# Kernel optimization log

Hardware: AMD Instinct MI355X
Metric: run time of the kernel (lower is better)

## Reference

```python
import jax, jax.numpy as jnp
import numpy as np

B, N, C, L, E = 8, 8192, 256, 4, 131072  # graphs, nodes/graph, channels (in=hidden=out), layers, edges/graph


def setup_inputs() -> dict:
    key = jax.random.key(0)
    ks = jax.random.split(key, 9)
    batch_node_tsr = jax.random.normal(ks[0], (B, N, C), jnp.float32)
    edge_index = jax.random.randint(ks[1], (B, 2, E), 0, N, jnp.int32)
    batch_last_node_idx_list = jnp.arange(1, B + 1, dtype=jnp.int32) * N - 1
    s1 = 1.0 / np.sqrt(C)
    s2 = 1.0 / np.sqrt(2 * C)
    # Base GraphConv layers: out = x @ Wr.T + sum_nbr(x) @ Wn.T + b  (all CxC since in=hidden=out)
    base_Wr = jax.random.uniform(ks[2], (L, C, C), jnp.float32, -s1, s1)
    base_Wn = jax.random.uniform(ks[3], (L, C, C), jnp.float32, -s1, s1)
    base_b = jax.random.uniform(ks[4], (L, C), jnp.float32, -s1, s1)
    # Adapter GraphConv layers take concatenated (2C) input
    adapt_Wr = jax.random.uniform(ks[5], (L, C, 2 * C), jnp.float32, -s2, s2)
    adapt_Wn = jax.random.uniform(ks[6], (L, C, 2 * C), jnp.float32, -s2, s2)
    adapt_b = jax.random.uniform(ks[7], (L, C), jnp.float32, -s2, s2)
    return dict(batch_node_tsr=batch_node_tsr, base_Wr=base_Wr, base_Wn=base_Wn,
                base_b=base_b, adapt_Wr=adapt_Wr, adapt_Wn=adapt_Wn, adapt_b=adapt_b,
                edge_index=edge_index, batch_last_node_idx_list=batch_last_node_idx_list)


def reference(batch_node_tsr, base_Wr, base_Wn, base_b, adapt_Wr, adapt_Wn, adapt_b,
              edge_index, batch_last_node_idx_list):
    # Batch graphs PyG-style: offset per-graph node indices into one big graph
    offsets = (jnp.arange(B, dtype=edge_index.dtype) * N)[:, None]  # [B,1]
    src = (edge_index[:, 0, :] + offsets).reshape(-1)  # [B*E]
    dst = (edge_index[:, 1, :] + offsets).reshape(-1)  # [B*E]
    x = batch_node_tsr.reshape(B * N, C)

    def gconv(h, Wr, Wn, b):
        # GraphConv: root transform + sum-aggregated neighbor transform
        agg = jax.ops.segment_sum(h[src], dst, num_segments=B * N)
        return h @ Wr.T + agg @ Wn.T + b

    # Base encoder pass, keeping all latent embeds
    lat = [x]
    for i in range(L):
        lat.append(jax.nn.relu(gconv(lat[-1], base_Wr[i], base_Wn[i], base_b[i])))
    base_batch_embed = lat[-1].reshape(B, N, C)

    # Adapter pass: concat(base_latent[i+1], curr) -> adapter GraphConv -> relu
    curr = x
    for i in range(L):
        curr = jax.nn.relu(gconv(jnp.concatenate([lat[i + 1], curr], axis=-1),
                                 adapt_Wr[i], adapt_Wn[i], adapt_b[i]))
    adapter_batch_embed = curr.reshape(B, N, C)
    return base_batch_embed, adapter_batch_embed
```

## Files before the change

kernel.cpp:

```cpp
#include <hip/hip_runtime.h>

#define B_ 8
#define N_ 8192
#define C_ 256
#define L_ 4
#define E_ 131072
#define BN_ 65536
#define EDGES_ 1048576
#define NKEY_ (BN_ * 4)

typedef __attribute__((ext_vector_type(8))) short short8;
typedef __attribute__((ext_vector_type(4))) float f32x4;

__device__ __forceinline__ unsigned short f2bf(float f){
  unsigned int u = __builtin_bit_cast(unsigned int, f);
  u += 0x7fffu + ((u >> 16) & 1u);
  return (unsigned short)(u >> 16);
}
__device__ __forceinline__ float bf2f(unsigned short h){
  unsigned int u = ((unsigned int)h) << 16;
  return __builtin_bit_cast(float, u);
}

__launch_bounds__(256)
__global__ void cvt_bf16_k(const float* __restrict__ in, unsigned short* __restrict__ out, int n4){
  int t = blockIdx.x * 256 + threadIdx.x;
  if (t >= n4) return;
  float4 v = ((const float4*)in)[t];
  ushort4 o;
  o.x = f2bf(v.x); o.y = f2bf(v.y); o.z = f2bf(v.z); o.w = f2bf(v.w);
  ((ushort4*)out)[t] = o;
}

__launch_bounds__(256)
__global__ void hist_k(const int* __restrict__ ei, int* __restrict__ cnt){
  int t = blockIdx.x * 256 + threadIdx.x;
  int b = t >> 17, e = t & (E_ - 1);
  int src = ei[b * (2 * E_) + e];
  int dst = ei[b * (2 * E_) + E_ + e];
  int key = (((b << 13) + dst) << 2) | (src >> 11);
  atomicAdd(&cnt[key], 1);
}

__launch_bounds__(256)
__global__ void scanA_k(const int* __restrict__ cnt, int* __restrict__ bsum){
  __shared__ int ls[256];
  int b = blockIdx.x, t = threadIdx.x;
  int4 v = *(const int4*)(cnt + b * 1024 + t * 4);
  int s = v.x + v.y + v.z + v.w;
  ls[t] = s;
  __syncthreads();
  for (int d = 128; d > 0; d >>= 1){
    if (t < d) ls[t] += ls[t + d];
    __syncthreads();
  }
  if (t == 0) bsum[b] = ls[0];
}
__launch_bounds__(256)
__global__ void scanB_k(const int* __restrict__ bsum, int* __restrict__ boff){
  __shared__ int ls[256];
  int t = threadIdx.x;
  int v = bsum[t];
  ls[t] = v;
  __syncthreads();
  for (int d = 1; d < 256; d <<= 1){
    int x = (t >= d) ? ls[t - d] : 0;
    __syncthreads();
    ls[t] += x;
    __syncthreads();
  }
  boff[t] = ls[t] - v;
}
__launch_bounds__(256)
__global__ void scanC_k(const int* __restrict__ cnt, const int* __restrict__ boff,
                        int* __restrict__ row_ptr, int* __restrict__ cursor){
  __shared__ int ls[256];
  int b = blockIdx.x, t = threadIdx.x;
  int base = b * 1024 + t * 4;
  int4 v = *(const int4*)(cnt + base);
  int s = v.x + v.y + v.z + v.w;
  ls[t] = s;
  __syncthreads();
  for (int d = 1; d < 256; d <<= 1){
    int x = (t >= d) ? ls[t - d] : 0;
    __syncthreads();
    ls[t] += x;
    __syncthreads();
  }
  int off = boff[b] + ls[t] - s;
  int4 rp;
  rp.x = off;
  rp.y = off + v.x;
  rp.z = rp.y + v.y;
  rp.w = rp.z + v.z;
  *(int4*)(row_ptr + base) = rp;
  *(int4*)(cursor + base) = rp;
  if (b == 255 && t == 255) row_ptr[NKEY_] = EDGES_;
}

__launch_bounds__(256)
__global__ void scat_k(const int* __restrict__ ei, int* __restrict__ cursor, int* __restrict__ col){
  int t = blockIdx.x * 256 + threadIdx.x;
  int b = t >> 17, e = t & (E_ - 1);
  int src = ei[b * (2 * E_) + e];
  int dst = ei[b * (2 * E_) + E_ + e];
  int key = (((b << 13) + dst) << 2) | (src >> 11);
  int pos = atomicAdd(&cursor[key], 1);
  col[pos] = (b << 13) + src;
}

__launch_bounds__(256)
__global__ void agg_k(const unsigned short* __restrict__ feat, const int* __restrict__ row_ptr,
                      const int* __restrict__ col, unsigned short* __restrict__ out){
  int w = threadIdx.x >> 6, lane = threadIdx.x & 63;
  int g = blockIdx.x & 7, sblk = blockIdx.x >> 3;
  int node = (g << 13) + (sblk << 2) + w;
  int beg = row_ptr[node << 2], end = row_ptr[(node << 2) + 4];
  int ch = lane << 2;
  float a0=0,a1=0,a2=0,a3=0;
  int e = beg;
  for (; e + 4 <= end; e += 4){
    int s0 = __builtin_nontemporal_load(col + e);
    int s1 = __builtin_nontemporal_load(col + e + 1);
    int s2 = __builtin_nontemporal_load(col + e + 2);
    int s3 = __builtin_nontemporal_load(col + e + 3);
    ushort4 v0 = *(const ushort4*)(feat + ((size_t)s0 << 8) + ch);
    ushort4 v1 = *(const ushort4*)(feat + ((size_t)s1 << 8) + ch);
    ushort4 v2 = *(const ushort4*)(feat + ((size_t)s2 << 8) + ch);
    ushort4 v3 = *(const ushort4*)(feat + ((size_t)s3 << 8) + ch);
    a0 += (bf2f(v0.x) + bf2f(v1.x)) + (bf2f(v2.x) + bf2f(v3.x));
    a1 += (bf2f(v0.y) + bf2f(v1.y)) + (bf2f(v2.y) + bf2f(v3.y));
    a2 += (bf2f(v0.z) + bf2f(v1.z)) + (bf2f(v2.z) + bf2f(v3.z));
    a3 += (bf2f(v0.w) + bf2f(v1.w)) + (bf2f(v2.w) + bf2f(v3.w));
  }
  for (; e < end; ++e){
    int s0 = __builtin_nontemporal_load(col + e);
    ushort4 v0 = *(const ushort4*)(feat + ((size_t)s0 << 8) + ch);
    a0 += bf2f(v0.x); a1 += bf2f(v0.y); a2 += bf2f(v0.z); a3 += bf2f(v0.w);
  }
  ushort4 o;
  o.x = f2bf(a0); o.y = f2bf(a1); o.z = f2bf(a2); o.w = f2bf(a3);
  unsigned long long ov = __builtin_bit_cast(unsigned long long, o);
  __builtin_nontemporal_store(ov, (unsigned long long*)(out + ((size_t)node << 8) + ch));
}

__launch_bounds__(256)
__global__ void agg2_k(const unsigned short* __restrict__ fA, const unsigned short* __restrict__ fB,
                       const int* __restrict__ row_ptr, const int* __restrict__ col,
                       unsigned short* __restrict__ oA, unsigned short* __restrict__ oB){
  int w = threadIdx.x >> 6, lane = threadIdx.x & 63;
  int g = blockIdx.x & 7, sblk = blockIdx.x >> 3;
  int node = (g << 13) + (sblk << 2) + w;
  int beg = row_ptr[node << 2], end = row_ptr[(node << 2) + 4];
  int ch = lane << 2;
  float a0=0,a1=0,a2=0,a3=0, c0=0,c1=0,c2=0,c3=0;
  int e = beg;
  for (; e + 2 <= end; e += 2){
    int s0 = __builtin_nontemporal_load(col + e);
    int s1 = __builtin_nontemporal_load(col + e + 1);
    ushort4 va0 = *(const ushort4*)(fA + ((size_t)s0 << 8) + ch);
    ushort4 vb0 = *(const ushort4*)(fB + ((size_t)s0 << 8) + ch);
    ushort4 va1 = *(const ushort4*)(fA + ((size_t)s1 << 8) + ch);
    ushort4 vb1 = *(const ushort4*)(fB + ((size_t)s1 << 8) + ch);
    a0 += bf2f(va0.x) + bf2f(va1.x); a1 += bf2f(va0.y) + bf2f(va1.y);
    a2 += bf2f(va0.z) + bf2f(va1.z); a3 += bf2f(va0.w) + bf2f(va1.w);
    c0 += bf2f(vb0.x) + bf2f(vb1.x); c1 += bf2f(vb0.y) + bf2f(vb1.y);
    c2 += bf2f(vb0.z) + bf2f(vb1.z); c3 += bf2f(vb0.w) + bf2f(vb1.w);
  }
  if (e < end){
    int s0 = __builtin_nontemporal_load(col + e);
    ushort4 va0 = *(const ushort4*)(fA + ((size_t)s0 << 8) + ch);
    ushort4 vb0 = *(const ushort4*)(fB + ((size_t)s0 << 8) + ch);
    a0 += bf2f(va0.x); a1 += bf2f(va0.y); a2 += bf2f(va0.z); a3 += bf2f(va0.w);
    c0 += bf2f(vb0.x); c1 += bf2f(vb0.y); c2 += bf2f(vb0.z); c3 += bf2f(vb0.w);
  }
  ushort4 oa, ob;
  oa.x = f2bf(a0); oa.y = f2bf(a1); oa.z = f2bf(a2); oa.w = f2bf(a3);
  ob.x = f2bf(c0); ob.y = f2bf(c1); ob.z = f2bf(c2); ob.w = f2bf(c3);
  unsigned long long va = __builtin_bit_cast(unsigned long long, oa);
  unsigned long long vb = __builtin_bit_cast(unsigned long long, ob);
  __builtin_nontemporal_store(va, (unsigned long long*)(oA + ((size_t)node << 8) + ch));
  __builtin_nontemporal_store(vb, (unsigned long long*)(oB + ((size_t)node << 8) + ch));
}

#define GLDS16(gp, lp) __builtin_amdgcn_global_load_lds( \
    (const __attribute__((address_space(1))) void*)(gp), \
    (__attribute__((address_space(3))) void*)(lp), 16, 0, 0)

__device__ __forceinline__ void stage_tiles(const unsigned short* __restrict__ A,
                                            const unsigned short* __restrict__ W,
                                            int ldw, int k0, unsigned short* a_t, int t){
  unsigned short* b_t = a_t + 4096;
#pragma unroll
  for (int c = t; c < 512; c += 256){
    int row = c >> 2, seg = c & 3;
    int sg = seg ^ ((row >> 1) & 3);
    GLDS16(A + row * C_  + k0 + sg * 8, &a_t[c * 8]);
  }
#pragma unroll
  for (int c = t; c < 1024; c += 256){
    int row = c >> 2, seg = c & 3;
    int sg = seg ^ ((row >> 1) & 3);
    GLDS16(W + row * ldw + k0 + sg * 8, &b_t[c * 8]);
  }
}

template<int P>
__launch_bounds__(256)
__global__ void gemm_k(const unsigned short* __restrict__ A0, const unsigned short* __restrict__ A1,
                       const unsigned short* __restrict__ A2, const unsigned short* __restrict__ A3,
                       const unsigned short* __restrict__ W0, const unsigned short* __restrict__ W1,
                       const unsigned short* __restrict__ W2, const unsigned short* __restrict__ W3,
                       int ldw, const float* __restrict__ bias,
                       unsigned short* __restrict__ outb, float* __restrict__ outf){
  __shared__ unsigned short lds_u[24576];
  const unsigned short* As[4] = {A0, A1, A2, A3};
  const unsigned short* Ws[4] = {W0, W1, W2, W3};
  const int m0 = blockIdx.x << 7;
  const int t = threadIdx.x, lane = t & 63;
  const int w = t >> 6;
  const int lrow = lane & 15, kg = lane >> 4;
  f32x4 acc[2][16] = {};

  stage_tiles(As[0] + (size_t)m0 * C_, Ws[0], ldw, 0, lds_u, t);
#pragma unroll
  for (int p = 0; p < P; ++p){
    const unsigned short* A = As[p] + (size_t)m0 * C_;
    const unsigned short* W = Ws[p];
#pragma unroll
    for (int ks = 0; ks < 8; ++ks){
      const int par = ks & 1;
      const bool more = (ks < 7) || (p + 1 < P);
      if (ks < 7)
        stage_tiles(A, W, ldw, (ks + 1) << 5, lds_u + (par ^ 1) * 12288, t);
      else if (p + 1 < P)
        stage_tiles(As[p + 1] + (size_t)m0 * C_, Ws[p + 1], ldw, 0, lds_u + (par ^ 1) * 12288, t);
      if (more) asm volatile("s_waitcnt vmcnt(6)" ::: "memory");
      else      asm volatile("s_waitcnt vmcnt(0)" ::: "memory");
      __builtin_amdgcn_s_barrier();
      const unsigned short* a_t = lds_u + par * 12288;
      const unsigned short* b_t = a_t + 4096;
      short8 af[2];
#pragma unroll
      for (int m = 0; m < 2; ++m){
        int ra = (w << 5) + (m << 4) + lrow;
        af[m] = *(const short8*)&a_t[ra * 32 + ((kg ^ ((ra >> 1) & 3)) << 3)];
      }
#pragma unroll
      for (int h = 0; h < 2; ++h){
        short8 bfr[8];
#pragma unroll
        for (int n2 = 0; n2 < 8; ++n2){
          int rb = (h << 7) + (n2 << 4) + lrow;
          bfr[n2] = *(const short8*)&b_t[rb * 32 + ((kg ^ ((rb >> 1) & 3)) << 3)];
        }
#pragma unroll
        for (int m = 0; m < 2; ++m)
#pragma unroll
          for (int n2 = 0; n2 < 8; ++n2)
            acc[m][(h << 3) + n2] =
                __builtin_amdgcn_mfma_f32_16x16x32_bf16(af[m], bfr[n2], acc[m][(h << 3) + n2], 0, 0, 0);
      }
      __builtin_amdgcn_s_barrier();
    }
  }
  float bv[16];
#pragma unroll
  for (int n = 0; n < 16; ++n) bv[n] = bias[(n << 4) + lrow];
  unsigned short* ep  = lds_u + (w << 11);
  float*          epf = (float*)(&lds_u[8192]) + (w << 11);
#pragma unroll
  for (int m = 0; m < 2; ++m){
    const int gr = m0 + (w << 5) + (m << 4);
    if (outf){
#pragma unroll
      for (int h = 0; h < 2; ++h){
#pragma unroll
        for (int n2 = 0; n2 < 8; ++n2){
          int n = (h << 3) + n2;
#pragma unroll
          for (int j = 0; j < 4; ++j){
            float v = acc[m][n][j] + bv[n];
            v = v > 0.f ? v : 0.f;
            epf[((kg << 2) + j) * 128 + (n2 << 4) + lrow] = v;
          }
        }
#pragma unroll
        for (int k = 0; k < 8; ++k){
          int r = (lane >> 5) + (k << 1);
          float4 v = *(const float4*)&epf[r * 128 + (lane & 31) * 4];
          *(float4*)&outf[(size_t)(gr + r) * C_ + (h << 7) + (lane & 31) * 4] = v;
        }
      }
    }
    if (outb){
#pragma unroll
      for (int h = 0; h < 2; ++h){
#pragma unroll
        for (int n2 = 0; n2 < 8; ++n2){
          int n = (h << 3) + n2;
#pragma unroll
          for (int j = 0; j < 4; ++j){
            float v = acc[m][n][j] + bv[n];
            v = v > 0.f ? v : 0.f;
            ep[((kg << 2) + j) * 128 + (n2 << 4) + lrow] = f2bf(v);
          }
        }
#pragma unroll
        for (int k = 0; k < 4; ++k){
          int r = (lane >> 4) + (k << 2);
          short8 v = *(const short8*)&ep[r * 128 + (lane & 15) * 8];
          *(short8*)&outb[(size_t)(gr + r) * C_ + (h << 7) + (lane & 15) * 8] = v;
        }
      }
    }
  }
}

extern "C" void kernel_launch(void* const* d_in, const int* in_sizes, int n_in,
                              void* d_out, int out_size, void* d_ws, size_t ws_size,
                              hipStream_t stream){
  const float* x_f   = (const float*)d_in[0];
  const float* bWr_f = (const float*)d_in[1];
  const float* bWn_f = (const float*)d_in[2];
  const float* bB    = (const float*)d_in[3];
  const float* aWr_f = (const float*)d_in[4];
  const float* aWn_f = (const float*)d_in[5];
  const float* aB    = (const float*)d_in[6];
  const int*   ei    = (const int*)d_in[7];
  float* out = (float*)d_out;
  (void)in_sizes; (void)n_in; (void)out_size; (void)ws_size;

  char* p = (char*)d_ws;
  const size_t BUF = (size_t)BN_ * C_ * sizeof(unsigned short);
  auto alloc = [&](size_t bytes){ void* r = (void*)p; p += (bytes + 255) & ~(size_t)255; return r; };
  unsigned short* xb   = (unsigned short*)alloc(BUF);
  unsigned short* latA = (unsigned short*)alloc(BUF);
  unsigned short* latB = (unsigned short*)alloc(BUF);
  unsigned short* curA = (unsigned short*)alloc(BUF);
  unsigned short* curB = (unsigned short*)alloc(BUF);
  unsigned short* agg0 = (unsigned short*)alloc(BUF);
  unsigned short* agg1 = (unsigned short*)alloc(BUF);
  unsigned short* wbR  = (unsigned short*)alloc((size_t)L_ * C_ * C_ * 2);
  unsigned short* wbN  = (unsigned short*)alloc((size_t)L_ * C_ * C_ * 2);
  unsigned short* waR  = (unsigned short*)alloc((size_t)L_ * C_ * 2 * C_ * 2);
  unsigned short* waN  = (unsigned short*)alloc((size_t)L_ * C_ * 2 * C_ * 2);
  int* cnt     = (int*)alloc((size_t)NKEY_ * 4);
  int* row_ptr = (int*)alloc((size_t)(NKEY_ + 1) * 4);
  int* cursor  = (int*)alloc((size_t)NKEY_ * 4);
  int* colx    = (int*)alloc((size_t)EDGES_ * 4);
  int* bsum    = (int*)alloc(256 * 4);
  int* boff    = (int*)alloc(256 * 4);

  cvt_bf16_k<<<BN_ * C_ / 4 / 256, 256, 0, stream>>>(x_f, xb, BN_ * C_ / 4);
  cvt_bf16_k<<<L_ * C_ * C_ / 4 / 256, 256, 0, stream>>>(bWr_f, wbR, L_ * C_ * C_ / 4);
  cvt_bf16_k<<<L_ * C_ * C_ / 4 / 256, 256, 0, stream>>>(bWn_f, wbN, L_ * C_ * C_ / 4);
  cvt_bf16_k<<<L_ * C_ * 2 * C_ / 4 / 256, 256, 0, stream>>>(aWr_f, waR, L_ * C_ * 2 * C_ / 4);
  cvt_bf16_k<<<L_ * C_ * 2 * C_ / 4 / 256, 256, 0, stream>>>(aWn_f, waN, L_ * C_ * 2 * C_ / 4);

  hipMemsetAsync(cnt, 0, (size_t)NKEY_ * 4, stream);
  hist_k<<<EDGES_ / 256, 256, 0, stream>>>(ei, cnt);
  scanA_k<<<256, 256, 0, stream>>>(cnt, bsum);
  scanB_k<<<1, 256, 0, stream>>>(bsum, boff);
  scanC_k<<<256, 256, 0, stream>>>(cnt, boff, row_ptr, cursor);
  scat_k<<<EDGES_ / 256, 256, 0, stream>>>(ei, cursor, colx);

  const int AGG_GRID  = BN_ / 4;
  const int GEMM_GRID = BN_ / 128;

  const size_t WB = (size_t)C_ * C_;
  const size_t WA = (size_t)C_ * 2 * C_;

  agg_k<<<AGG_GRID, 256, 0, stream>>>(xb, row_ptr, colx, agg0);
  gemm_k<2><<<GEMM_GRID, 256, 0, stream>>>(xb, agg0, nullptr, nullptr,
      wbR, wbN, nullptr, nullptr, C_, bB, latA, nullptr);
  agg_k<<<AGG_GRID, 256, 0, stream>>>(latA, row_ptr, colx, agg1);
  gemm_k<2><<<GEMM_GRID, 256, 0, stream>>>(latA, agg1, nullptr, nullptr,
      wbR + WB, wbN + WB, nullptr, nullptr, C_, bB + 256, latB, nullptr);
  gemm_k<4><<<GEMM_GRID, 256, 0, stream>>>(latA, xb, agg1, agg0,
      waR, waR + 256, waN, waN + 256, 2 * C_, aB, curA, nullptr);
  agg2_k<<<AGG_GRID, 256, 0, stream>>>(latB, curA, row_ptr, colx, agg1, agg0);
  gemm_k<2><<<GEMM_GRID, 256, 0, stream>>>(latB, agg1, nullptr, nullptr,
      wbR + 2 * WB, wbN + 2 * WB, nullptr, nullptr, C_, bB + 512, latA, nullptr);
  gemm_k<4><<<GEMM_GRID, 256, 0, stream>>>(latB, curA, agg1, agg0,
      waR + WA, waR + WA + 256, waN + WA, waN + WA + 256, 2 * C_, aB + 256, curB, nullptr);
  agg2_k<<<AGG_GRID, 256, 0, stream>>>(latA, curB, row_ptr, colx, agg1, agg0);
  gemm_k<2><<<GEMM_GRID, 256, 0, stream>>>(latA, agg1, nullptr, nullptr,
      wbR + 3 * WB, wbN + 3 * WB, nullptr, nullptr, C_, bB + 768, latB, out);
  gemm_k<4><<<GEMM_GRID, 256, 0, stream>>>(latA, curB, agg1, agg0,
      waR + 2 * WA, waR + 2 * WA + 256, waN + 2 * WA, waN + 2 * WA + 256, 2 * C_, aB + 512, curA, nullptr);
  agg2_k<<<AGG_GRID, 256, 0, stream>>>(latB, curA, row_ptr, colx, agg1, agg0);
  gemm_k<4><<<GEMM_GRID, 256, 0, stream>>>(latB, curA, agg1, agg0,
      waR + 3 * WA, waR + 3 * WA + 256, waN + 3 * WA, waN + 3 * WA + 256, 2 * C_, aB + 768,
      nullptr, out + (size_t)BN_ * C_);
}
```

Measured before the change: 1.152 ms.

## Split aggregation across channel slices and shrink GEMM tile to 64 rows

The aggregation kernels now split the channel dimension across extra blocks: agg_k uses two halves with 2-channel loads, and agg2_k uses four quarters with scalar loads. Each edge loop is unrolled 8-wide to keep more gathers in flight. The GEMM drops from 128-row to 64-row tiles with a 4x4 MFMA accumulator per wave, uses less LDS, raises launch bounds to 4 blocks per CU, and rewrites the epilogue around full-row LDS staging. The aim is higher occupancy and more parallelism, at the cost of narrower, less coalesced gather loads, repeated index reads per channel slice, and more reloading of the weight tile across blocks.

```diff
diff --git a/kernel.cpp b/kernel.cpp
--- a/kernel.cpp
+++ b/kernel.cpp
@@ -113,35 +113,31 @@
 __global__ void agg_k(const unsigned short* __restrict__ feat, const int* __restrict__ row_ptr,
                       const int* __restrict__ col, unsigned short* __restrict__ out){
   int w = threadIdx.x >> 6, lane = threadIdx.x & 63;
-  int g = blockIdx.x & 7, sblk = blockIdx.x >> 3;
+  int h = blockIdx.x >> 14;
+  int inner = blockIdx.x & 16383;
+  int g = inner & 7, sblk = inner >> 3;
   int node = (g << 13) + (sblk << 2) + w;
   int beg = row_ptr[node << 2], end = row_ptr[(node << 2) + 4];
-  int ch = lane << 2;
-  float a0=0,a1=0,a2=0,a3=0;
+  int ch = (h << 7) + (lane << 1);
+  float a0 = 0.f, a1 = 0.f;
   int e = beg;
-  for (; e + 4 <= end; e += 4){
-    int s0 = __builtin_nontemporal_load(col + e);
-    int s1 = __builtin_nontemporal_load(col + e + 1);
-    int s2 = __builtin_nontemporal_load(col + e + 2);
-    int s3 = __builtin_nontemporal_load(col + e + 3);
-    ushort4 v0 = *(const ushort4*)(feat + ((size_t)s0 << 8) + ch);
-    ushort4 v1 = *(const ushort4*)(feat + ((size_t)s1 << 8) + ch);
-    ushort4 v2 = *(const ushort4*)(feat + ((size_t)s2 << 8) + ch);
-    ushort4 v3 = *(const ushort4*)(feat + ((size_t)s3 << 8) + ch);
-    a0 += (bf2f(v0.x) + bf2f(v1.x)) + (bf2f(v2.x) + bf2f(v3.x));
-    a1 += (bf2f(v0.y) + bf2f(v1.y)) + (bf2f(v2.y) + bf2f(v3.y));
-    a2 += (bf2f(v0.z) + bf2f(v1.z)) + (bf2f(v2.z) + bf2f(v3.z));
-    a3 += (bf2f(v0.w) + bf2f(v1.w)) + (bf2f(v2.w) + bf2f(v3.w));
+  for (; e + 8 <= end; e += 8){
+    int s[8]; ushort2 v[8];
+#pragma unroll
+    for (int i = 0; i < 8; ++i) s[i] = col[e + i];
+#pragma unroll
+    for (int i = 0; i < 8; ++i) v[i] = *(const ushort2*)(feat + ((size_t)s[i] << 8) + ch);
+#pragma unroll
+    for (int i = 0; i < 8; ++i){ a0 += bf2f(v[i].x); a1 += bf2f(v[i].y); }
   }
   for (; e < end; ++e){
-    int s0 = __builtin_nontemporal_load(col + e);
-    ushort4 v0 = *(const ushort4*)(feat + ((size_t)s0 << 8) + ch);
-    a0 += bf2f(v0.x); a1 += bf2f(v0.y); a2 += bf2f(v0.z); a3 += bf2f(v0.w);
-  }
-  ushort4 o;
-  o.x = f2bf(a0); o.y = f2bf(a1); o.z = f2bf(a2); o.w = f2bf(a3);
-  unsigned long long ov = __builtin_bit_cast(unsigned long long, o);
-  __builtin_nontemporal_store(ov, (unsigned long long*)(out + ((size_t)node << 8) + ch));
+    int s0 = col[e];
+    ushort2 v0 = *(const ushort2*)(feat + ((size_t)s0 << 8) + ch);
+    a0 += bf2f(v0.x); a1 += bf2f(v0.y);
+  }
+  ushort2 o;
+  o.x = f2bf(a0); o.y = f2bf(a1);
+  *(ushort2*)(out + ((size_t)node << 8) + ch) = o;
 }
 
 __launch_bounds__(256)
@@ -149,38 +145,33 @@
                        const int* __restrict__ row_ptr, const int* __restrict__ col,
                        unsigned short* __restrict__ oA, unsigned short* __restrict__ oB){
   int w = threadIdx.x >> 6, lane = threadIdx.x & 63;
-  int g = blockIdx.x & 7, sblk = blockIdx.x >> 3;
+  int q = blockIdx.x >> 14;
+  int inner = blockIdx.x & 16383;
+  int g = inner & 7, sblk = inner >> 3;
   int node = (g << 13) + (sblk << 2) + w;
   int beg = row_ptr[node << 2], end = row_ptr[(node << 2) + 4];
-  int ch = lane << 2;
-  float a0=0,a1=0,a2=0,a3=0, c0=0,c1=0,c2=0,c3=0;
+  int ch = (q << 6) + lane;
+  float a = 0.f, c = 0.f;
   int e = beg;
-  for (; e + 2 <= end; e += 2){
-    int s0 = __builtin_nontemporal_load(col + e);
-    int s1 = __builtin_nontemporal_load(col + e + 1);
-    ushort4 va0 = *(const ushort4*)(fA + ((size_t)s0 << 8) + ch);
-    ushort4 vb0 = *(const ushort4*)(fB + ((size_t)s0 << 8) + ch);
-    ushort4 va1 = *(const ushort4*)(fA + ((size_t)s1 << 8) + ch);
-    ushort4 vb1 = *(const ushort4*)(fB + ((size_t)s1 << 8) + ch);
-    a0 += bf2f(va0.x) + bf2f(va1.x); a1 += bf2f(va0.y) + bf2f(va1.y);
-    a2 += bf2f(va0.z) + bf2f(va1.z); a3 += bf2f(va0.w) + bf2f(va1.w);
-    c0 += bf2f(vb0.x) + bf2f(vb1.x); c1 += bf2f(vb0.y) + bf2f(vb1.y);
-    c2 += bf2f(vb0.z) + bf2f(vb1.z); c3 += bf2f(vb0.w) + bf2f(vb1.w);
-  }
-  if (e < end){
-    int s0 = __builtin_nontemporal_load(col + e);
-    ushort4 va0 = *(const ushort4*)(fA + ((size_t)s0 << 8) + ch);
-    ushort4 vb0 = *(const ushort4*)(fB + ((size_t)s0 << 8) + ch);
-    a0 += bf2f(va0.x); a1 += bf2f(va0.y); a2 += bf2f(va0.z); a3 += bf2f(va0.w);
-    c0 += bf2f(vb0.x); c1 += bf2f(vb0.y); c2 += bf2f(vb0.z); c3 += bf2f(vb0.w);
-  }
-  ushort4 oa, ob;
-  oa.x = f2bf(a0); oa.y = f2bf(a1); oa.z = f2bf(a2); oa.w = f2bf(a3);
-  ob.x = f2bf(c0); ob.y = f2bf(c1); ob.z = f2bf(c2); ob.w = f2bf(c3);
-  unsigned long long va = __builtin_bit_cast(unsigned long long, oa);
-  unsigned long long vb = __builtin_bit_cast(unsigned long long, ob);
-  __builtin_nontemporal_store(va, (unsigned long long*)(oA + ((size_t)node << 8) + ch));
-  __builtin_nontemporal_store(vb, (unsigned long long*)(oB + ((size_t)node << 8) + ch));
+  for (; e + 8 <= end; e += 8){
+    int s[8]; unsigned short va[8], vb[8];
+#pragma unroll
+    for (int i = 0; i < 8; ++i) s[i] = col[e + i];
+#pragma unroll
+    for (int i = 0; i < 8; ++i){
+      va[i] = fA[((size_t)s[i] << 8) + ch];
+      vb[i] = fB[((size_t)s[i] << 8) + ch];
+    }
+#pragma unroll
+    for (int i = 0; i < 8; ++i){ a += bf2f(va[i]); c += bf2f(vb[i]); }
+  }
+  for (; e < end; ++e){
+    int s0 = col[e];
+    a += bf2f(fA[((size_t)s0 << 8) + ch]);
+    c += bf2f(fB[((size_t)s0 << 8) + ch]);
+  }
+  oA[((size_t)node << 8) + ch] = f2bf(a);
+  oB[((size_t)node << 8) + ch] = f2bf(c);
 }
 
 #define GLDS16(gp, lp) __builtin_amdgcn_global_load_lds( \
@@ -190,15 +181,15 @@
 __device__ __forceinline__ void stage_tiles(const unsigned short* __restrict__ A,
                                             const unsigned short* __restrict__ W,
                                             int ldw, int k0, unsigned short* a_t, int t){
-  unsigned short* b_t = a_t + 4096;
-#pragma unroll
-  for (int c = t; c < 512; c += 256){
-    int row = c >> 2, seg = c & 3;
+  unsigned short* b_t = a_t + 2048;
+  {
+    int row = t >> 2, seg = t & 3;
     int sg = seg ^ ((row >> 1) & 3);
-    GLDS16(A + row * C_  + k0 + sg * 8, &a_t[c * 8]);
-  }
-#pragma unroll
-  for (int c = t; c < 1024; c += 256){
+    GLDS16(A + row * C_ + k0 + sg * 8, &a_t[t * 8]);
+  }
+#pragma unroll
+  for (int i = 0; i < 4; ++i){
+    int c = t + i * 256;
     int row = c >> 2, seg = c & 3;
     int sg = seg ^ ((row >> 1) & 3);
     GLDS16(W + row * ldw + k0 + sg * 8, &b_t[c * 8]);
@@ -206,21 +197,21 @@
 }
 
 template<int P>
-__launch_bounds__(256)
+__launch_bounds__(256, 4)
 __global__ void gemm_k(const unsigned short* __restrict__ A0, const unsigned short* __restrict__ A1,
                        const unsigned short* __restrict__ A2, const unsigned short* __restrict__ A3,
                        const unsigned short* __restrict__ W0, const unsigned short* __restrict__ W1,
                        const unsigned short* __restrict__ W2, const unsigned short* __restrict__ W3,
                        int ldw, const float* __restrict__ bias,
                        unsigned short* __restrict__ outb, float* __restrict__ outf){
-  __shared__ unsigned short lds_u[24576];
+  __shared__ unsigned short lds_u[20480];
   const unsigned short* As[4] = {A0, A1, A2, A3};
   const unsigned short* Ws[4] = {W0, W1, W2, W3};
-  const int m0 = blockIdx.x << 7;
+  const int m0 = blockIdx.x << 6;
   const int t = threadIdx.x, lane = t & 63;
   const int w = t >> 6;
   const int lrow = lane & 15, kg = lane >> 4;
-  f32x4 acc[2][16] = {};
+  f32x4 acc[4][4] = {};
 
   stage_tiles(As[0] + (size_t)m0 * C_, Ws[0], ldw, 0, lds_u, t);
 #pragma unroll
@@ -232,87 +223,85 @@
       const int par = ks & 1;
       const bool more = (ks < 7) || (p + 1 < P);
       if (ks < 7)
-        stage_tiles(A, W, ldw, (ks + 1) << 5, lds_u + (par ^ 1) * 12288, t);
+        stage_tiles(A, W, ldw, (ks + 1) << 5, lds_u + (par ^ 1) * 10240, t);
       else if (p + 1 < P)
-        stage_tiles(As[p + 1] + (size_t)m0 * C_, Ws[p + 1], ldw, 0, lds_u + (par ^ 1) * 12288, t);
-      if (more) asm volatile("s_waitcnt vmcnt(6)" ::: "memory");
+        stage_tiles(As[p + 1] + (size_t)m0 * C_, Ws[p + 1], ldw, 0, lds_u + (par ^ 1) * 10240, t);
+      if (more) asm volatile("s_waitcnt vmcnt(5)" ::: "memory");
       else      asm volatile("s_waitcnt vmcnt(0)" ::: "memory");
       __builtin_amdgcn_s_barrier();
-      const unsigned short* a_t = lds_u + par * 12288;
-      const unsigned short* b_t = a_t + 4096;
-      short8 af[2];
-#pragma unroll
-      for (int m = 0; m < 2; ++m){
-        int ra = (w << 5) + (m << 4) + lrow;
+      const unsigned short* a_t = lds_u + par * 10240;
+      const unsigned short* b_t = a_t + 2048;
+      short8 af[4];
+#pragma unroll
+      for (int m = 0; m < 4; ++m){
+        int ra = (m << 4) + lrow;
         af[m] = *(const short8*)&a_t[ra * 32 + ((kg ^ ((ra >> 1) & 3)) << 3)];
       }
 #pragma unroll
-      for (int h = 0; h < 2; ++h){
-        short8 bfr[8];
-#pragma unroll
-        for (int n2 = 0; n2 < 8; ++n2){
-          int rb = (h << 7) + (n2 << 4) + lrow;
-          bfr[n2] = *(const short8*)&b_t[rb * 32 + ((kg ^ ((rb >> 1) & 3)) << 3)];
-        }
-#pragma unroll
-        for (int m = 0; m < 2; ++m)
-#pragma unroll
-          for (int n2 = 0; n2 < 8; ++n2)
-            acc[m][(h << 3) + n2] =
-                __builtin_amdgcn_mfma_f32_16x16x32_bf16(af[m], bfr[n2], acc[m][(h << 3) + n2], 0, 0, 0);
+      for (int n = 0; n < 4; ++n){
+        int rb = (w << 6) + (n << 4) + lrow;
+        short8 bfr = *(const short8*)&b_t[rb * 32 + ((kg ^ ((rb >> 1) & 3)) << 3)];
+#pragma unroll
+        for (int m = 0; m < 4; ++m)
+          acc[m][n] = __builtin_amdgcn_mfma_f32_16x16x32_bf16(af[m], bfr, acc[m][n], 0, 0, 0);
       }
       __builtin_amdgcn_s_barrier();
     }
   }
-  float bv[16];
-#pragma unroll
-  for (int n = 0; n < 16; ++n) bv[n] = bias[(n << 4) + lrow];
-  unsigned short* ep  = lds_u + (w << 11);
-  float*          epf = (float*)(&lds_u[8192]) + (w << 11);
-#pragma unroll
-  for (int m = 0; m < 2; ++m){
-    const int gr = m0 + (w << 5) + (m << 4);
-    if (outf){
-#pragma unroll
-      for (int h = 0; h < 2; ++h){
-#pragma unroll
-        for (int n2 = 0; n2 < 8; ++n2){
-          int n = (h << 3) + n2;
-#pragma unroll
-          for (int j = 0; j < 4; ++j){
-            float v = acc[m][n][j] + bv[n];
-            v = v > 0.f ? v : 0.f;
-            epf[((kg << 2) + j) * 128 + (n2 << 4) + lrow] = v;
-          }
+  float bv[4];
+#pragma unroll
+  for (int n = 0; n < 4; ++n) bv[n] = bias[(w << 6) + (n << 4) + lrow];
+  if (outb){
+    unsigned short* eb = lds_u;
+#pragma unroll
+    for (int m = 0; m < 4; ++m)
+#pragma unroll
+      for (int n = 0; n < 4; ++n)
+#pragma unroll
+        for (int j = 0; j < 4; ++j){
+          int row = (m << 4) + (kg << 2) + j;
+          int c0 = (w << 6) + (n << 4) + lrow;
+          float v = acc[m][n][j] + bv[n];
+          v = v > 0.f ? v : 0.f;
+          eb[row * 264 + c0] = f2bf(v);
         }
-#pragma unroll
-        for (int k = 0; k < 8; ++k){
-          int r = (lane >> 5) + (k << 1);
-          float4 v = *(const float4*)&epf[r * 128 + (lane & 31) * 4];
-          *(float4*)&outf[(size_t)(gr + r) * C_ + (h << 7) + (lane & 31) * 4] = v;
-        }
+    __syncthreads();
+#pragma unroll
+    for (int s = 0; s < 8; ++s){
+      int flat8 = s * 256 + t;
+      int row = flat8 >> 5, col8 = flat8 & 31;
+      short8 v = *(const short8*)&eb[row * 264 + col8 * 8];
+      *(short8*)&outb[(size_t)(m0 + row) * C_ + col8 * 8] = v;
+    }
+    if (outf) __syncthreads();
+  }
+  if (outf){
+    float* ef = (float*)lds_u;
+#pragma unroll
+    for (int h = 0; h < 2; ++h){
+      if ((w >> 1) == h){
+#pragma unroll
+        for (int m = 0; m < 4; ++m)
+#pragma unroll
+          for (int n = 0; n < 4; ++n)
+#pragma unroll
+            for (int j = 0; j < 4; ++j){
+              int row = (m << 4) + (kg << 2) + j;
+              int ch = ((w & 1) << 6) + (n << 4) + lrow;
+              float v = acc[m][n][j] + bv[n];
+              v = v > 0.f ? v : 0.f;
+              ef[row * 132 + ch] = v;
+            }
       }
-    }
-    if (outb){
-#pragma unroll
-      for (int h = 0; h < 2; ++h){
-#pragma unroll
-        for (int n2 = 0; n2 < 8; ++n2){
-          int n = (h << 3) + n2;
-#pragma unroll
-          for (int j = 0; j < 4; ++j){
-            float v = acc[m][n][j] + bv[n];
-            v = v > 0.f ? v : 0.f;
-            ep[((kg << 2) + j) * 128 + (n2 << 4) + lrow] = f2bf(v);
-          }
-        }
-#pragma unroll
-        for (int k = 0; k < 4; ++k){
-          int r = (lane >> 4) + (k << 2);
-          short8 v = *(const short8*)&ep[r * 128 + (lane & 15) * 8];
-          *(short8*)&outb[(size_t)(gr + r) * C_ + (h << 7) + (lane & 15) * 8] = v;
-        }
+      __syncthreads();
+#pragma unroll
+      for (int s = 0; s < 8; ++s){
+        int flat4 = s * 256 + t;
+        int row = flat4 >> 5, col4 = flat4 & 31;
+        float4 v = *(const float4*)&ef[row * 132 + col4 * 4];
+        *(float4*)&outf[(size_t)(m0 + row) * C_ + (h << 7) + col4 * 4] = v;
       }
+      if (h == 0) __syncthreads();
     }
   }
 }
@@ -365,8 +354,9 @@
   scanC_k<<<256, 256, 0, stream>>>(cnt, boff, row_ptr, cursor);
   scat_k<<<EDGES_ / 256, 256, 0, stream>>>(ei, cursor, colx);
 
-  const int AGG_GRID  = BN_ / 4;
-  const int GEMM_GRID = BN_ / 128;
+  const int AGG_GRID  = 2 * 16384;
+  const int AGG2_GRID = 4 * 16384;
+  const int GEMM_GRID = BN_ / 64;
 
   const size_t WB = (size_t)C_ * C_;
   const size_t WA = (size_t)C_ * 2 * C_;
@@ -379,17 +369,17 @@
       wbR + WB, wbN + WB, nullptr, nullptr, C_, bB + 256, latB, nullptr);
   gemm_k<4><<<GEMM_GRID, 256, 0, stream>>>(latA, xb, agg1, agg0,
       waR, waR + 256, waN, waN + 256, 2 * C_, aB, curA, nullptr);
-  agg2_k<<<AGG_GRID, 256, 0, stream>>>(latB, curA, row_ptr, colx, agg1, agg0);
+  agg2_k<<<AGG2_GRID, 256, 0, stream>>>(latB, curA, row_ptr, colx, agg1, agg0);
   gemm_k<2><<<GEMM_GRID, 256, 0, stream>>>(latB, agg1, nullptr, nullptr,
       wbR + 2 * WB, wbN + 2 * WB, nullptr, nullptr, C_, bB + 512, latA, nullptr);
   gemm_k<4><<<GEMM_GRID, 256, 0, stream>>>(latB, curA, agg1, agg0,
       waR + WA, waR + WA + 256, waN + WA, waN + WA + 256, 2 * C_, aB + 256, curB, nullptr);
-  agg2_k<<<AGG_GRID, 256, 0, stream>>>(latA, curB, row_ptr, colx, agg1, agg0);
+  agg2_k<<<AGG2_GRID, 256, 0, stream>>>(latA, curB, row_ptr, colx, agg1, agg0);
   gemm_k<2><<<GEMM_GRID, 256, 0, stream>>>(latA, agg1, nullptr, nullptr,
       wbR + 3 * WB, wbN + 3 * WB, nullptr, nullptr, C_, bB + 768, latB, out);
   gemm_k<4><<<GEMM_GRID, 256, 0, stream>>>(latA, curB, agg1, agg0,
       waR + 2 * WA, waR + 2 * WA + 256, waN + 2 * WA, waN + 2 * WA + 256, 2 * C_, aB + 512, curA, nullptr);
-  agg2_k<<<AGG_GRID, 256, 0, stream>>>(latB, curA, row_ptr, colx, agg1, agg0);
+  agg2_k<<<AGG2_GRID, 256, 0, stream>>>(latB, curA, row_ptr, colx, agg1, agg0);
   gemm_k<4><<<GEMM_GRID, 256, 0, stream>>>(latB, curA, agg1, agg0,
       waR + 3 * WA, waR + 3 * WA + 256, waN + 3 * WA, waN + 3 * WA + 256, 2 * C_, aB + 768,
       nullptr, out + (size_t)BN_ * C_);
```

New measurement: 1.157 ms. No clear change (+0.4%).
